# Performance work log

Measured on AMD Instinct MI355X. Metric: run time of the kernel, lower is better.

## Reference

```python
import jax, jax.numpy as jnp
import numpy as np

B, D, K, A, P = 4096, 512, 128, 32, 16  # batch, theta dim, mixture comps, alpha dim, hutchinson probes


def setup_inputs() -> dict:
    key = jax.random.key(0)
    k1, k2, k3, k4 = jax.random.split(key, 4)
    thetas = jax.random.normal(k1, (B, D), dtype=jnp.float32)
    alpha = jax.random.normal(k2, (K, A), dtype=jnp.float32)
    W = jax.random.normal(k3, (A, D), dtype=jnp.float32) / jnp.sqrt(jnp.float32(A))
    v_int = jax.random.randint(k4, (P, B, D), 0, 2, dtype=jnp.int32)  # -> Rademacher via 2v-1
    return {"thetas": thetas, "alpha": alpha, "W": W, "v_int": v_int,
            "N_dataset": 100000, "K_alpha_samples": K}


def _log_density(thetas, alpha, W, N_dataset, K_alpha):
    # Tempered Gaussian mixture: mu_k = alpha_k @ W;
    # logp_b = (N/(N+1)) * (logsumexp_k -0.5||theta_b - mu_k||^2 - log K)
    mu = alpha @ W                                        # [K, D]
    # ||t - mu||^2 expanded to avoid a [B,K,D] intermediate
    sq = (jnp.sum(thetas * thetas, -1, keepdims=True)
          - 2.0 * thetas @ mu.T
          + jnp.sum(mu * mu, -1)[None, :])                # [B, K]
    temper = jnp.float32(N_dataset) / (jnp.float32(N_dataset) + 1.0)
    return temper * (jax.nn.logsumexp(-0.5 * sq, axis=1) - jnp.log(jnp.float32(K_alpha)))


def reference(thetas, alpha, W, v_int, N_dataset, K_alpha_samples):
    v = (2 * v_int - 1).astype(thetas.dtype)              # [P, B, D] Rademacher

    def logp_sum(t):
        return jnp.sum(_log_density(t, alpha, W, N_dataset, K_alpha_samples))

    score = jax.grad(logp_sum)                            # gradiente wrt thetas
    g = score(thetas)                                     # [B, D]

    # Hutchinson trace of the per-sample Hessian via forward-over-reverse HVPs,
    # batched over probes (fuses the torch per-probe autograd.grad loop).
    def hvp(vi):
        return jax.jvp(score, (thetas,), (vi,))[1]        # [B, D]

    Hv = jax.vmap(hvp)(v)                                 # [P, B, D]
    traces = jnp.mean(jnp.sum(v * Hv, axis=-1), axis=0)   # [B]

    loss = 0.5 * jnp.sum(g * g, axis=-1) + traces         # [B]
    return jnp.mean(loss)
```

## Files before the change

kernel.cpp:

```cpp
#include <hip/hip_runtime.h>
#include <hip/hip_bf16.h>
#include <stdint.h>

#define Bsz 4096
#define Dn  512
#define Kn  128
#define Pn  16
#define An  32
#define TB  16

typedef __attribute__((ext_vector_type(4))) float  floatx4;
typedef __attribute__((ext_vector_type(8))) short  shortx8;

__device__ unsigned short g_mu_bf[Kn * Dn];
__device__ unsigned short g_mu_t[Dn * Kn];
__device__ float          g_munorm[Kn];
__device__ float          g_w[Bsz * Kn];

__device__ __forceinline__ unsigned short f2bf(float x) {
    union { float f; uint32_t u; } v; v.f = x;
    uint32_t u = v.u;
    uint32_t r = (u + 0x7FFFu + ((u >> 16) & 1u)) >> 16;
    return (unsigned short)r;
}

__device__ __forceinline__ float rowsum16(float x) {
    x += __int_as_float(__builtin_amdgcn_update_dpp(0, __float_as_int(x), 0xB1, 0xF, 0xF, false));
    x += __int_as_float(__builtin_amdgcn_update_dpp(0, __float_as_int(x), 0x4E, 0xF, 0xF, false));
    x += __int_as_float(__builtin_amdgcn_update_dpp(0, __float_as_int(x), 0x124, 0xF, 0xF, false));
    x += __int_as_float(__builtin_amdgcn_update_dpp(0, __float_as_int(x), 0x128, 0xF, 0xF, false));
    return x;
}

__global__ __launch_bounds__(256) void k_mu(const float* __restrict__ alpha,
                                            const float* __restrict__ W,
                                            float* __restrict__ out) {
    __shared__ float al[An];
    __shared__ float red[4];
    int k = blockIdx.x, t = threadIdx.x;
    if (k == 0 && t == 0) *out = 0.f;
    if (t < An) al[t] = alpha[k * An + t];
    __syncthreads();
    int d0 = t, d1 = t + 256;
    float a0 = 0.f, a1 = 0.f;
#pragma unroll
    for (int a = 0; a < An; ++a) {
        float av = al[a];
        a0 = fmaf(av, W[a * Dn + d0], a0);
        a1 = fmaf(av, W[a * Dn + d1], a1);
    }
    unsigned short h0 = f2bf(a0), h1 = f2bf(a1);
    g_mu_bf[k * Dn + d0] = h0;  g_mu_bf[k * Dn + d1] = h1;
    g_mu_t[d0 * Kn + k] = h0;   g_mu_t[d1 * Kn + k] = h1;
    float nrm = a0 * a0 + a1 * a1;
#pragma unroll
    for (int msk = 1; msk < 64; msk <<= 1) nrm += __shfl_xor(nrm, msk);
    if ((t & 63) == 0) red[t >> 6] = nrm;
    __syncthreads();
    if (t == 0) g_munorm[k] = red[0] + red[1] + red[2] + red[3];
}

__global__ __launch_bounds__(512) void k_w(const float* __restrict__ thetas,
                                           const int* __restrict__ Np,
                                           float* __restrict__ out) {
    __shared__ short vt[TB][520];
    __shared__ float S_l[TB][132];
    __shared__ float w_l[TB][132];
    __shared__ short wbf[TB][136];
    __shared__ float part8[8][TB];
    __shared__ float thn[TB];
    __shared__ float SwS[TB];

    const int tid = threadIdx.x;
    const int lane = tid & 63;
    const int wv = tid >> 6;
    const int m = lane & 15;
    const int q = lane >> 4;
    const int b0 = blockIdx.x * TB;

    const float Nf = (float)(*Np);
    const float temper = Nf / (Nf + 1.0f);

    const int kcol = wv * 16 + m;
    shortx8 mufrag[16];
    {
        const unsigned short* mb = g_mu_bf + (size_t)kcol * Dn + q * 8;
#pragma unroll
        for (int dc = 0; dc < 16; ++dc)
            mufrag[dc] = *(const shortx8*)(mb + dc * 32);
    }

    const int r = tid >> 5;
    const int c0 = (tid & 31) * 16;
    {
        const float4* tg = (const float4*)(thetas + (size_t)(b0 + r) * Dn + c0);
        float tn = 0.f;
#pragma unroll
        for (int j = 0; j < 4; ++j) {
            float4 f = tg[j];
            tn += f.x * f.x + f.y * f.y + f.z * f.z + f.w * f.w;
            short4 h;
            h.x = (short)f2bf(f.x); h.y = (short)f2bf(f.y);
            h.z = (short)f2bf(f.z); h.w = (short)f2bf(f.w);
            *(short4*)&vt[r][c0 + j * 4] = h;
        }
#pragma unroll
        for (int msk = 1; msk < 32; msk <<= 1) tn += __shfl_xor(tn, msk);
        if ((tid & 31) == 0) thn[r] = tn;
    }
    __syncthreads();

    {
        floatx4 acc = {0.f, 0.f, 0.f, 0.f};
#pragma unroll
        for (int dc = 0; dc < 16; ++dc) {
            shortx8 a = *(const shortx8*)&vt[m][dc * 32 + q * 8];
            acc = __builtin_amdgcn_mfma_f32_16x16x32_bf16(a, mufrag[dc], acc, 0, 0, 0);
        }
#pragma unroll
        for (int i = 0; i < 4; ++i) S_l[q * 4 + i][kcol] = acc[i];
    }
    __syncthreads();

    {
        const int b = tid >> 5, s = tid & 31;
        float l[4];
        float mx = -3.4e38f;
        float tnb = thn[b];
#pragma unroll
        for (int j = 0; j < 4; ++j) {
            int k = s + 32 * j;
            l[j] = -0.5f * (tnb - 2.f * S_l[b][k] + g_munorm[k]);
            mx = fmaxf(mx, l[j]);
        }
#pragma unroll
        for (int msk = 1; msk < 32; msk <<= 1) mx = fmaxf(mx, __shfl_xor(mx, msk));
        float se = 0.f, ses = 0.f;
        float e[4];
#pragma unroll
        for (int j = 0; j < 4; ++j) {
            int k = s + 32 * j;
            e[j] = __expf(l[j] - mx);
            se += e[j];
            ses += e[j] * S_l[b][k];
        }
#pragma unroll
        for (int msk = 1; msk < 32; msk <<= 1) { se += __shfl_xor(se, msk); ses += __shfl_xor(ses, msk); }
        float inv = 1.f / se;
#pragma unroll
        for (int j = 0; j < 4; ++j) {
            int k = s + 32 * j;
            float wvv = e[j] * inv;
            w_l[b][k] = wvv;
            wbf[b][k] = (short)f2bf(wvv);
            g_w[(size_t)(b0 + b) * Kn + k] = wvv;
        }
        if (s == 0) SwS[b] = ses * inv;
    }
    __syncthreads();

    {
        float sg[4] = {0.f, 0.f, 0.f, 0.f};
#pragma unroll
        for (int ct = 0; ct < 4; ++ct) {
            const unsigned short* mt = g_mu_t + (size_t)(wv * 64 + ct * 16 + m) * Kn + q * 8;
            floatx4 acc = {0.f, 0.f, 0.f, 0.f};
#pragma unroll
            for (int kc = 0; kc < 4; ++kc) {
                shortx8 a = *(const shortx8*)&wbf[m][kc * 32 + q * 8];
                shortx8 bfr = *(const shortx8*)(mt + kc * 32);
                acc = __builtin_amdgcn_mfma_f32_16x16x32_bf16(a, bfr, acc, 0, 0, 0);
            }
#pragma unroll
            for (int i = 0; i < 4; ++i) sg[i] += acc[i] * acc[i];
        }
#pragma unroll
        for (int i = 0; i < 4; ++i) sg[i] = rowsum16(sg[i]);
        if (m == 0) {
#pragma unroll
            for (int i = 0; i < 4; ++i) part8[wv][q * 4 + i] = sg[i];
        }
    }
    __syncthreads();

    if (tid < TB) {
        float wGw = 0.f;
#pragma unroll
        for (int w8 = 0; w8 < 8; ++w8) wGw += part8[w8][tid];
        float res = 0.5f * temper * temper * (wGw - 2.f * SwS[tid] + thn[tid])
                    - temper * (float)Dn;
#pragma unroll
        for (int msk = 1; msk < 16; msk <<= 1) res += __shfl_xor(res, msk);
        if (tid == 0) atomicAdd(out, res * (1.0f / (float)Bsz));
    }
}

__global__ __launch_bounds__(512, 4) void k_probe(const int* __restrict__ v_int,
                                                  const int* __restrict__ Np,
                                                  float* __restrict__ out) {
    __shared__ float partial[8];

    const int tid = threadIdx.x;
    const int lane = tid & 63;
    const int w = tid >> 6;
    const int m = lane & 15;
    const int q = lane >> 4;

    const int bid = blockIdx.x;
    const int probe = bid >> 5;
    const int btile = bid & 31;
    const int r0 = btile * 128 + w * 16;

    const float Nf = (float)(*Np);
    const float temper = Nf / (Nf + 1.0f);

    const size_t PB = (size_t)Bsz * Dn;
    const char* vg = (const char*)(v_int + (size_t)probe * PB + (size_t)(r0 + m) * Dn) + q * 32;
    const unsigned short* mub = g_mu_bf + (size_t)m * Dn + q * 8;

    int4 vb[4][2];
#pragma unroll
    for (int c = 0; c < 4; ++c) {
        vb[c][0] = *(const int4*)(vg + c * 128);
        vb[c][1] = *(const int4*)(vg + c * 128 + 16);
    }

    floatx4 acc[8];
#pragma unroll
    for (int kt = 0; kt < 8; ++kt) acc[kt] = (floatx4){0.f, 0.f, 0.f, 0.f};

#pragma unroll
    for (int dc = 0; dc < 16; ++dc) {
        int4 w0 = vb[dc & 3][0], w1 = vb[dc & 3][1];
        if (dc < 12) {
            vb[dc & 3][0] = *(const int4*)(vg + (dc + 4) * 128);
            vb[dc & 3][1] = *(const int4*)(vg + (dc + 4) * 128 + 16);
        }
        union { uint32_t u[4]; shortx8 s; } af;
        af.u[0] = 0xBF80BF80u ^ ((uint32_t)w0.x << 15) ^ ((uint32_t)w0.y << 31);
        af.u[1] = 0xBF80BF80u ^ ((uint32_t)w0.z << 15) ^ ((uint32_t)w0.w << 31);
        af.u[2] = 0xBF80BF80u ^ ((uint32_t)w1.x << 15) ^ ((uint32_t)w1.y << 31);
        af.u[3] = 0xBF80BF80u ^ ((uint32_t)w1.z << 15) ^ ((uint32_t)w1.w << 31);
#pragma unroll
        for (int kt = 0; kt < 8; ++kt) {
            shortx8 bf = *(const shortx8*)(mub + (size_t)kt * 16 * Dn + dc * 32);
            acc[kt] = __builtin_amdgcn_mfma_f32_16x16x32_bf16(af.s, bf, acc[kt], 0, 0, 0);
        }
    }

    float contrib = 0.f;
#pragma unroll
    for (int i = 0; i < 4; ++i) {
        const float* wrow = g_w + (size_t)(r0 + q * 4 + i) * Kn + m;
        float s1 = 0.f, s2 = 0.f;
#pragma unroll
        for (int kt = 0; kt < 8; ++kt) {
            float T = acc[kt][i];
            float ww = wrow[kt * 16];
            s1 = fmaf(ww * T, T, s1);
            s2 = fmaf(ww, T, s2);
        }
        s1 = rowsum16(s1);
        s2 = rowsum16(s2);
        contrib += s1 - s2 * s2;
    }
    if (m != 0) contrib = 0.f;
    contrib += __shfl_xor(contrib, 16);
    contrib += __shfl_xor(contrib, 32);
    if (lane == 0) partial[w] = contrib;
    __syncthreads();
    if (tid == 0) {
        float t = 0.f;
#pragma unroll
        for (int i = 0; i < 8; ++i) t += partial[i];
        atomicAdd(out, t * temper * (1.0f / (float)Pn) * (1.0f / (float)Bsz));
    }
}

extern "C" void kernel_launch(void* const* d_in, const int* in_sizes, int n_in,
                              void* d_out, int out_size, void* d_ws, size_t ws_size,
                              hipStream_t stream) {
    const float* thetas = (const float*)d_in[0];
    const float* alpha  = (const float*)d_in[1];
    const float* W      = (const float*)d_in[2];
    const int*   v_int  = (const int*)d_in[3];
    const int*   Np     = (const int*)d_in[4];
    (void)d_ws; (void)ws_size;

    float* out = (float*)d_out;
    k_mu   <<<dim3(Kn),  dim3(256), 0, stream>>>(alpha, W, out);
    k_w    <<<dim3(256), dim3(512), 0, stream>>>(thetas, Np, out);
    k_probe<<<dim3(512), dim3(512), 0, stream>>>(v_int, Np, out);
}
```

Measured before the change: 255.1 us.

## Stage bf16 mu and w rows in swizzled LDS, one block per row tile

k_probe now stages the whole bf16 mu matrix (128 KB) into XOR-swizzled shared memory, plus the 16-row w tile, once per block. It then remaps the grid so each 1024-thread block handles one 16-row batch tile, with its 16 waves covering the 16 probes. The MFMA B operands come from LDS instead of repeated global/L2 reads, and the w loads are shared across probes. The 128 KB LDS footprint limits occupancy to about one block per CU, and the 256-block grid is a single wave with an up-front staging cost.

New measurement: 223.2 us. 1.14x faster.

```diff
diff --git a/kernel.cpp b/kernel.cpp
--- a/kernel.cpp
+++ b/kernel.cpp
@@ -195,28 +195,44 @@
     }
 }
 
-__global__ __launch_bounds__(512, 4) void k_probe(const int* __restrict__ v_int,
-                                                  const int* __restrict__ Np,
-                                                  float* __restrict__ out) {
-    __shared__ float partial[8];
+__global__ __launch_bounds__(1024, 4) void k_probe(const int* __restrict__ v_int,
+                                                   const int* __restrict__ Np,
+                                                   float* __restrict__ out) {
+    __shared__ __align__(16) unsigned short mu_l[Kn * Dn];
+    __shared__ float w_l[TB][132];
+    __shared__ float partial[16];
 
     const int tid = threadIdx.x;
     const int lane = tid & 63;
-    const int w = tid >> 6;
+    const int wv = tid >> 6;
     const int m = lane & 15;
     const int q = lane >> 4;
-
-    const int bid = blockIdx.x;
-    const int probe = bid >> 5;
-    const int btile = bid & 31;
-    const int r0 = btile * 128 + w * 16;
+    const int bt = blockIdx.x;
+    const int r0 = bt * TB;
 
     const float Nf = (float)(*Np);
     const float temper = Nf / (Nf + 1.0f);
 
+    {
+        const int4* src = (const int4*)g_mu_bf;
+#pragma unroll
+        for (int i = 0; i < 8; ++i) {
+            int c = i * 1024 + tid;
+            int row = c >> 6;
+            int off = (c & 63) * 16;
+            int4 val = src[c];
+            *(int4*)((char*)mu_l + row * 1024 + (off ^ ((row & 7) << 4))) = val;
+        }
+    }
+    if (tid < 512) {
+        int row = tid >> 5, c = (tid & 31) * 4;
+        float4 w4 = *(const float4*)(g_w + (size_t)(r0 + row) * Kn + c);
+        *(float4*)&w_l[row][c] = w4;
+    }
+    __syncthreads();
+
     const size_t PB = (size_t)Bsz * Dn;
-    const char* vg = (const char*)(v_int + (size_t)probe * PB + (size_t)(r0 + m) * Dn) + q * 32;
-    const unsigned short* mub = g_mu_bf + (size_t)m * Dn + q * 8;
+    const char* vg = (const char*)(v_int + (size_t)wv * PB + (size_t)(r0 + m) * Dn) + q * 32;
 
     int4 vb[4][2];
 #pragma unroll
@@ -229,6 +245,7 @@
 #pragma unroll
     for (int kt = 0; kt < 8; ++kt) acc[kt] = (floatx4){0.f, 0.f, 0.f, 0.f};
 
+    const int swz = (m & 7) << 4;
 #pragma unroll
     for (int dc = 0; dc < 16; ++dc) {
         int4 w0 = vb[dc & 3][0], w1 = vb[dc & 3][1];
@@ -241,9 +258,11 @@
         af.u[1] = 0xBF80BF80u ^ ((uint32_t)w0.z << 15) ^ ((uint32_t)w0.w << 31);
         af.u[2] = 0xBF80BF80u ^ ((uint32_t)w1.x << 15) ^ ((uint32_t)w1.y << 31);
         af.u[3] = 0xBF80BF80u ^ ((uint32_t)w1.z << 15) ^ ((uint32_t)w1.w << 31);
+        const int boff = dc * 64 + q * 16;
 #pragma unroll
         for (int kt = 0; kt < 8; ++kt) {
-            shortx8 bf = *(const shortx8*)(mub + (size_t)kt * 16 * Dn + dc * 32);
+            shortx8 bf = *(const shortx8*)((const char*)mu_l
+                              + (kt * 16 + m) * 1024 + (boff ^ swz));
             acc[kt] = __builtin_amdgcn_mfma_f32_16x16x32_bf16(af.s, bf, acc[kt], 0, 0, 0);
         }
     }
@@ -251,12 +270,11 @@
     float contrib = 0.f;
 #pragma unroll
     for (int i = 0; i < 4; ++i) {
-        const float* wrow = g_w + (size_t)(r0 + q * 4 + i) * Kn + m;
         float s1 = 0.f, s2 = 0.f;
 #pragma unroll
         for (int kt = 0; kt < 8; ++kt) {
             float T = acc[kt][i];
-            float ww = wrow[kt * 16];
+            float ww = w_l[q * 4 + i][kt * 16 + m];
             s1 = fmaf(ww * T, T, s1);
             s2 = fmaf(ww, T, s2);
         }
@@ -267,12 +285,12 @@
     if (m != 0) contrib = 0.f;
     contrib += __shfl_xor(contrib, 16);
     contrib += __shfl_xor(contrib, 32);
-    if (lane == 0) partial[w] = contrib;
+    if (lane == 0) partial[wv] = contrib;
     __syncthreads();
     if (tid == 0) {
         float t = 0.f;
 #pragma unroll
-        for (int i = 0; i < 8; ++i) t += partial[i];
+        for (int i = 0; i < 16; ++i) t += partial[i];
         atomicAdd(out, t * temper * (1.0f / (float)Pn) * (1.0f / (float)Bsz));
     }
 }
@@ -288,7 +306,7 @@
     (void)d_ws; (void)ws_size;
 
     float* out = (float*)d_out;
-    k_mu   <<<dim3(Kn),  dim3(256), 0, stream>>>(alpha, W, out);
-    k_w    <<<dim3(256), dim3(512), 0, stream>>>(thetas, Np, out);
-    k_probe<<<dim3(512), dim3(512), 0, stream>>>(v_int, Np, out);
-}
+    k_mu   <<<dim3(Kn),  dim3(256),  0, stream>>>(alpha, W, out);
+    k_w    <<<dim3(256), dim3(512),  0, stream>>>(thetas, Np, out);
+    k_probe<<<dim3(256), dim3(1024), 0, stream>>>(v_int, Np, out);
+}
```
